# Optimization experiments

Hardware: AMD Instinct MI355X
Metric: run time of the kernel (lower is better)

The kernel has to match this reference:

```python
import jax, jax.numpy as jnp
import numpy as np

E, B, T, N, DIN = 8, 1024, 64, 16, 8
H, Z = 512, 128
DFLAT = T * N * DIN  # 8192


def setup_inputs() -> dict:
    key = jax.random.key(0)
    ks = jax.random.split(key, 10)
    def w(k, shape, fan_in):
        return jax.random.normal(k, shape, jnp.float32) * (1.0 / np.sqrt(fan_in))
    return {
        'x': jax.random.normal(ks[0], (B, T, N, DIN), jnp.float32),
        'eps': jax.random.normal(ks[1], (E, B, Z), jnp.float32),
        'enc_w1': w(ks[2], (E, DFLAT, H), DFLAT), 'enc_b1': jnp.zeros((E, H), jnp.float32),
        'enc_w2': w(ks[3], (E, H, H), H),         'enc_b2': jnp.zeros((E, H), jnp.float32),
        'mu_w':   w(ks[4], (E, H, Z), H),         'mu_b':   jnp.zeros((E, Z), jnp.float32),
        'lv_w':   w(ks[5], (E, H, Z), H),         'lv_b':   jnp.zeros((E, Z), jnp.float32),
        'dec_w1': w(ks[6], (E, Z, H), Z),         'dec_b1': jnp.zeros((E, H), jnp.float32),
        'dec_w2': w(ks[7], (E, H, H), H),         'dec_b2': jnp.zeros((E, H), jnp.float32),
        'dec_w3': w(ks[8], (E, H, DFLAT), H),     'dec_b3': jnp.zeros((E, DFLAT), jnp.float32),
    }


def _all_experts(x, eps, enc_w1, enc_b1, enc_w2, enc_b2, mu_w, mu_b, lv_w, lv_b,
                 dec_w1, dec_b1, dec_w2, dec_b2, dec_w3, dec_b3):
    # 'everyone_try_this_problem': every expert runs densely on the full batch.
    xf = x.reshape(x.shape[0], -1)                                            # [B, D]
    h = jax.nn.relu(jnp.einsum('bd,edh->ebh', xf, enc_w1) + enc_b1[:, None])  # [E, B, H]
    h = jax.nn.relu(jnp.einsum('ebh,ehk->ebk', h, enc_w2) + enc_b2[:, None])
    mu = jnp.einsum('ebh,ehz->ebz', h, mu_w) + mu_b[:, None]                  # [E, B, Z]
    logvar = jnp.einsum('ebh,ehz->ebz', h, lv_w) + lv_b[:, None]
    z = mu + jnp.exp(0.5 * logvar) * eps                                      # reparameterized sample
    hd = jax.nn.relu(jnp.einsum('ebz,ezh->ebh', z, dec_w1) + dec_b1[:, None])
    hd = jax.nn.relu(jnp.einsum('ebh,ehk->ebk', hd, dec_w2) + dec_b2[:, None])
    xhat = jnp.einsum('ebh,ehd->ebd', hd, dec_w3) + dec_b3[:, None]           # [E, B, D]
    losses = jnp.mean((xhat - xf[None]) ** 2, axis=-1)                        # [E, B] per-sample recon loss
    return mu, logvar, xhat, losses


def reference(x, eps, enc_w1, enc_b1, enc_w2, enc_b2, mu_w, mu_b, lv_w, lv_b,
              dec_w1, dec_b1, dec_w2, dec_b2, dec_w3, dec_b3):
    mu, logvar, xhat, losses = _all_experts(
        x, eps, enc_w1, enc_b1, enc_w2, enc_b2, mu_w, mu_b, lv_w, lv_b,
        dec_w1, dec_b1, dec_w2, dec_b2, dec_w3, dec_b3)
    # torch.min(all_loss[B,E], dim=1) -> argmin over experts (first-index tiebreak)
    expert_idx = jnp.argmin(losses, axis=0)                                   # [B]
    b = jnp.arange(x.shape[0])
    mu_sel = mu[expert_idx, b]                                                # [B, Z]
    logvar_sel = logvar[expert_idx, b]
    xhat_sel = xhat[expert_idx, b].reshape(x.shape)                           # [B, T, N, DIN]
    return mu_sel, logvar_sel, xhat_sel, expert_idx
```

## Files before the change

### kernel.cpp

```cpp
#include <hip/hip_runtime.h>

#define EE 8
#define BB 1024
#define DD 8192
#define HH 512
#define ZZ 128

typedef __attribute__((ext_vector_type(8))) short bf16x8;
typedef __attribute__((ext_vector_type(4))) float f32x4;
typedef __attribute__((address_space(1))) unsigned int u32g;
typedef __attribute__((address_space(3))) unsigned int u32l;

#define DEVI __device__ __forceinline__

DEVI float4 ld4(const float* p) { return *(const float4*)p; }

DEVI unsigned f2bf_u(float x) {
  unsigned u = __builtin_bit_cast(unsigned, x);
  return (u + 0x7FFFu + ((u >> 16) & 1u)) >> 16;
}
DEVI float bfu2f(unsigned h) { return __builtin_bit_cast(float, h << 16); }
DEVI float bf2f(short s) {
  return __builtin_bit_cast(float, ((unsigned)(unsigned short)s) << 16);
}
DEVI void split2(float x, short& hi, short& lo) {
  unsigned h = f2bf_u(x);
  hi = (short)h;
  lo = (short)f2bf_u(x - bfu2f(h));
}

DEVI void gload16(const void* g, void* l) {
  __builtin_amdgcn_global_load_lds((const u32g*)g, (u32l*)l, 16, 0, 0);
}

template <int ROWS, int WAVES>
DEVI void stageG(const short* src, int Kb, short* lds, int w, int laneoff) {
  const char* p = (const char*)src + laneoff;
  char* l = (char*)lds + w * 1024;
#pragma unroll
  for (int r = 0; r < ROWS / (WAVES * 8); ++r)
    gload16(p + (size_t)r * (WAVES * 8) * Kb, l + r * (WAVES * 1024));
}

template <int NPASS, int NF>
DEVI void mma_chunk(const char* Ah, const char* Al, const char* Bh, const char* Bl,
                    int abase, int bbase, f32x4 acc[4][NF]) {
#pragma unroll
  for (int kk = 0; kk < 2; ++kk) {
    const int kx = kk * 64;
    bf16x8 ah[4], al[4], bh[NF], bl[NF];
#pragma unroll
    for (int m = 0; m < 4; ++m) {
      ah[m] = *(const bf16x8*)(Ah + ((abase + m * 2048) ^ kx));
      if (NPASS == 3) al[m] = *(const bf16x8*)(Al + ((abase + m * 2048) ^ kx));
    }
#pragma unroll
    for (int n = 0; n < NF; ++n) {
      bh[n] = *(const bf16x8*)(Bh + ((bbase + n * 2048) ^ kx));
      if (NPASS == 3) bl[n] = *(const bf16x8*)(Bl + ((bbase + n * 2048) ^ kx));
    }
#pragma unroll
    for (int m = 0; m < 4; ++m)
#pragma unroll
      for (int n = 0; n < NF; ++n) {
        acc[m][n] = __builtin_amdgcn_mfma_f32_16x16x32_bf16(ah[m], bh[n], acc[m][n], 0, 0, 0);
        if (NPASS == 3) {
          acc[m][n] = __builtin_amdgcn_mfma_f32_16x16x32_bf16(ah[m], bl[n], acc[m][n], 0, 0, 0);
          acc[m][n] = __builtin_amdgcn_mfma_f32_16x16x32_bf16(al[m], bh[n], acc[m][n], 0, 0, 0);
        }
      }
  }
}

DEVI void mma_chunk256(const char* A, const char* B, int abase, int bbase,
                       f32x4 acc[8][4]) {
#pragma unroll
  for (int kk = 0; kk < 2; ++kk) {
    const int kx = kk * 64;
    bf16x8 ah[8], bh[4];
#pragma unroll
    for (int m = 0; m < 8; ++m) ah[m] = *(const bf16x8*)(A + ((abase + m * 2048) ^ kx));
#pragma unroll
    for (int n = 0; n < 4; ++n) bh[n] = *(const bf16x8*)(B + ((bbase + n * 2048) ^ kx));
#pragma unroll
    for (int m = 0; m < 8; ++m)
#pragma unroll
      for (int n = 0; n < 4; ++n)
        acc[m][n] = __builtin_amdgcn_mfma_f32_16x16x32_bf16(ah[m], bh[n], acc[m][n], 0, 0, 0);
  }
}

template <int NPASS, int NF, bool RELU, int OUT>
__global__ __launch_bounds__(256, (NPASS == 3 ? 2 : 3)) void gemm_k(
    const short* __restrict__ Ahg, const short* __restrict__ Alg,
    const short* __restrict__ Bhg, const short* __restrict__ Blg,
    const float* __restrict__ bias,
    float* __restrict__ Yf, short* __restrict__ Yh, short* __restrict__ Yl,
    int M, int N, int K, int APE, const int* __restrict__ cntPtr, int mSkip) {
  constexpr int BN = NF * 32;
  __shared__ short sA[(NPASS == 3 ? 2 : 1) * 128 * 64];
  __shared__ short sB[(NPASS == 3 ? 2 : 1) * BN * 64];
  const int e = blockIdx.z;
  const int m0 = blockIdx.y * 128, n0 = blockIdx.x * BN;
  if (m0 < mSkip) return;
  if (cntPtr) {
    if (m0 >= ((cntPtr[0] + 127) & ~127)) return;
  }
  const size_t eA = APE ? (size_t)e * M * K : 0;
  const short* Ae = Ahg + eA + (size_t)m0 * K;
  const short* Ale = (NPASS == 3) ? (Alg + eA + (size_t)m0 * K) : nullptr;
  const short* Be = Bhg + ((size_t)e * N + n0) * K;
  const short* Ble = (NPASS == 3) ? (Blg + ((size_t)e * N + n0) * K) : nullptr;

  const int t = threadIdx.x, w = t >> 6, lane = t & 63;
  const int wm = w >> 1, wn = w & 1;
  const int Kb = K * 2;
  const int laneoff = (w * 8 + (lane >> 3)) * Kb + (((lane & 7) ^ ((lane >> 3) & 7)) << 4);
  const int r16 = lane & 15, g = lane >> 4;
  const int c0 = ((g ^ (r16 & 7)) << 4);
  const int abase = (wm * 64 + r16) * 128 + c0;
  const int bbase = (wn * (NF * 16) + r16) * 128 + c0;

  f32x4 acc[4][NF];
#pragma unroll
  for (int m = 0; m < 4; ++m)
#pragma unroll
    for (int n = 0; n < NF; ++n) acc[m][n] = (f32x4){0.f, 0.f, 0.f, 0.f};

  for (int k0 = 0; k0 < K; k0 += 64) {
    stageG<128, 4>(Ae + k0, Kb, sA, w, laneoff);
    if (NPASS == 3) stageG<128, 4>(Ale + k0, Kb, sA + 128 * 64, w, laneoff);
    stageG<BN, 4>(Be + k0, Kb, sB, w, laneoff);
    if (NPASS == 3) stageG<BN, 4>(Ble + k0, Kb, sB + BN * 64, w, laneoff);
    __syncthreads();
    mma_chunk<NPASS, NF>((const char*)sA, (const char*)(sA + 128 * 64),
                         (const char*)sB, (const char*)(sB + BN * 64), abase, bbase, acc);
    __syncthreads();
  }

  const int col0 = n0 + wn * (NF * 16);
#pragma unroll
  for (int n = 0; n < NF; ++n) {
    const int cn = col0 + n * 16 + r16;
    const float bv = bias[(size_t)e * N + cn];
#pragma unroll
    for (int m = 0; m < 4; ++m)
#pragma unroll
      for (int r = 0; r < 4; ++r) {
        const int row = m0 + wm * 64 + m * 16 + g * 4 + r;
        float v = acc[m][n][r] + bv;
        if (RELU) v = fmaxf(v, 0.f);
        const size_t o = ((size_t)e * M + row) * N + cn;
        if (OUT == 0) {
          Yf[o] = v;
        } else {
          unsigned hb = f2bf_u(v);
          Yh[o] = (short)hb;
          if (NPASS == 3) Yl[o] = (short)f2bf_u(v - bfu2f(hb));
        }
      }
  }
}

__global__ __launch_bounds__(256, 4) void enc1_mainsplit_k(
    const short* __restrict__ Xhg, const short* __restrict__ Bhg,
    float* __restrict__ EncP) {
  __shared__ short sA[128 * 64];
  __shared__ short sB[64 * 64];
  const int raw = blockIdx.x;
  const int e = raw & 7;
  const int q = raw >> 3;
  const int m0 = (q & 7) * 128;
  const int ks = (q >> 3) & 1;
  const int n0 = (q >> 4) * 64;
  const int Kb = DD * 2;
  const short* Ae = Xhg + (size_t)m0 * DD;
  const short* Be = Bhg + ((size_t)e * HH + n0) * DD;

  const int t = threadIdx.x, w = t >> 6, lane = t & 63;
  const int wm = w >> 1, wn = w & 1;
  const int laneoff = (w * 8 + (lane >> 3)) * Kb + (((lane & 7) ^ ((lane >> 3) & 7)) << 4);
  const int r16 = lane & 15, g = lane >> 4;
  const int c0 = ((g ^ (r16 & 7)) << 4);
  const int abase = (wm * 64 + r16) * 128 + c0;
  const int bbase = (wn * 32 + r16) * 128 + c0;

  f32x4 acc[4][2];
#pragma unroll
  for (int m = 0; m < 4; ++m)
#pragma unroll
    for (int n = 0; n < 2; ++n) acc[m][n] = (f32x4){0.f, 0.f, 0.f, 0.f};

  const int kbeg = ks * 4096, kend = kbeg + 4096;
  for (int k0 = kbeg; k0 < kend; k0 += 64) {
    stageG<128, 4>(Ae + k0, Kb, sA, w, laneoff);
    stageG<64, 4>(Be + k0, Kb, sB, w, laneoff);
    __syncthreads();
    mma_chunk<1, 2>((const char*)sA, nullptr, (const char*)sB, nullptr,
                    abase, bbase, acc);
    __syncthreads();
  }

#pragma unroll
  for (int n = 0; n < 2; ++n) {
    const int cn = n0 + wn * 32 + n * 16 + r16;
#pragma unroll
    for (int m = 0; m < 4; ++m)
#pragma unroll
      for (int r = 0; r < 4; ++r) {
        const int row = m0 + wm * 64 + m * 16 + g * 4 + r;
        EncP[(((size_t)ks * EE + e) * BB + row) * HH + cn] = acc[m][n][r];
      }
  }
}

__global__ void fuse_enc1main_k(const float* __restrict__ EncP,
                                const float* __restrict__ enc_b1,
                                short* __restrict__ Hh) {
  const int idx = blockIdx.x * 256 + threadIdx.x;
  const size_t base = (size_t)idx * 8;
  float s[8];
  *(float4*)&s[0] = *(const float4*)&EncP[base];
  *(float4*)&s[4] = *(const float4*)&EncP[base + 4];
  {
    const float* p = EncP + (size_t)(EE * BB * HH) + base;
    float q[8];
    *(float4*)&q[0] = *(const float4*)p;
    *(float4*)&q[4] = *(const float4*)(p + 4);
#pragma unroll
    for (int j = 0; j < 8; ++j) s[j] += q[j];
  }
  const int e = (int)(base / (BB * HH));
  const int col = (int)(base % HH);
  short h8[8];
#pragma unroll
  for (int j = 0; j < 8; ++j) {
    const float v = fmaxf(s[j] + enc_b1[e * HH + col + j], 0.f);
    h8[j] = (short)f2bf_u(v);
  }
  *(bf16x8*)&Hh[base] = *(bf16x8*)h8;
}

__global__ __launch_bounds__(512, 2) void gemm_loss256_k(
    const short* __restrict__ Ahg, const short* __restrict__ Bhg,
    const float* __restrict__ bias, const short* __restrict__ xfh,
    float* __restrict__ partials) {
  __shared__ short sA[256 * 64];
  __shared__ short sB[256 * 64];
  __shared__ float red[256][4];
  int lin = blockIdx.x + 32 * (blockIdx.y + 4 * blockIdx.z);
  lin = (lin & 7) * 128 + (lin >> 3);
  const int bx = lin & 31, by = (lin >> 5) & 3, e = lin >> 7;
  const int m0 = by * 256, n0 = bx * 256;
  const int K = HH, Kb = HH * 2;
  const short* Ae = Ahg + ((size_t)e * BB + m0) * K;
  const short* Be = Bhg + ((size_t)e * DD + n0) * K;

  const int t = threadIdx.x, w = t >> 6, lane = t & 63;
  const int wm = w >> 2, wn = w & 3;
  const int laneoff = (w * 8 + (lane >> 3)) * Kb + (((lane & 7) ^ ((lane >> 3) & 7)) << 4);
  const int r16 = lane & 15, g = lane >> 4;
  const int c0 = ((g ^ (r16 & 7)) << 4);
  const int abase = (wm * 128 + r16) * 128 + c0;
  const int bbase = (wn * 64 + r16) * 128 + c0;

  f32x4 acc[8][4];
#pragma unroll
  for (int m = 0; m < 8; ++m)
#pragma unroll
    for (int n = 0; n < 4; ++n) acc[m][n] = (f32x4){0.f, 0.f, 0.f, 0.f};

  for (int k0 = 0; k0 < K; k0 += 64) {
    stageG<256, 8>(Ae + k0, Kb, sA, w, laneoff);
    stageG<256, 8>(Be + k0, Kb, sB, w, laneoff);
    __syncthreads();
    mma_chunk256((const char*)sA, (const char*)sB, abase, bbase, acc);
    __syncthreads();
  }

  float rs[8][4];
#pragma unroll
  for (int m = 0; m < 8; ++m)
#pragma unroll
    for (int r = 0; r < 4; ++r) rs[m][r] = 0.f;
#pragma unroll
  for (int n = 0; n < 4; ++n) {
    const int cn = n0 + wn * 64 + n * 16 + r16;
    const float bv = bias[(size_t)e * DD + cn];
#pragma unroll
    for (int m = 0; m < 8; ++m)
#pragma unroll
      for (int r = 0; r < 4; ++r) {
        const int row = m0 + wm * 128 + m * 16 + g * 4 + r;
        const float d = acc[m][n][r] + bv - bf2f(xfh[(size_t)row * DD + cn]);
        rs[m][r] = fmaf(d, d, rs[m][r]);
      }
  }
#pragma unroll
  for (int off = 1; off < 16; off <<= 1)
#pragma unroll
    for (int m = 0; m < 8; ++m)
#pragma unroll
      for (int r = 0; r < 4; ++r) rs[m][r] += __shfl_xor(rs[m][r], off);
  if (r16 == 0) {
#pragma unroll
    for (int m = 0; m < 8; ++m)
#pragma unroll
      for (int r = 0; r < 4; ++r) red[wm * 128 + m * 16 + g * 4 + r][wn] = rs[m][r];
  }
  __syncthreads();
  if (t < 256)
    partials[((size_t)e * BB + m0 + t) * 32 + bx] =
        red[t][0] + red[t][1] + red[t][2] + red[t][3];
}

template <int NPASS>
__global__ __launch_bounds__(256, 2) void gemm_loss_k(
    const short* __restrict__ Ahg, const short* __restrict__ Alg,
    const short* __restrict__ Bhg, const short* __restrict__ Blg,
    const float* __restrict__ bias, const float* __restrict__ xf,
    const int* __restrict__ rows, const int* __restrict__ cntPtr,
    float* __restrict__ partials, int K) {
  constexpr int NF = 4;
  __shared__ short sA[2 * 128 * 64];
  __shared__ short sB[2 * 128 * 64];
  __shared__ float red[128][2];
  const int e = blockIdx.z;
  const int m0 = blockIdx.y * 128, n0 = blockIdx.x * 128;
  int cntA = BB;
  if (cntPtr) {
    cntA = cntPtr[0];
    if (m0 >= ((cntA + 127) & ~127)) return;
  }
  const short* Ae = Ahg + ((size_t)e * BB + m0) * K;
  const short* Ale = Alg + ((size_t)e * BB + m0) * K;
  const short* Be = Bhg + ((size_t)e * DD + n0) * K;
  const short* Ble = Blg + ((size_t)e * DD + n0) * K;

  const int t = threadIdx.x, w = t >> 6, lane = t & 63;
  const int wm = w >> 1, wn = w & 1;
  const int Kb = K * 2;
  const int laneoff = (w * 8 + (lane >> 3)) * Kb + (((lane & 7) ^ ((lane >> 3) & 7)) << 4);
  const int r16 = lane & 15, g = lane >> 4;
  const int c0 = ((g ^ (r16 & 7)) << 4);
  const int abase = (wm * 64 + r16) * 128 + c0;
  const int bbase = (wn * 64 + r16) * 128 + c0;

  f32x4 acc[4][NF];
#pragma unroll
  for (int m = 0; m < 4; ++m)
#pragma unroll
    for (int n = 0; n < NF; ++n) acc[m][n] = (f32x4){0.f, 0.f, 0.f, 0.f};

  for (int k0 = 0; k0 < K; k0 += 64) {
    stageG<128, 4>(Ae + k0, Kb, sA, w, laneoff);
    stageG<128, 4>(Ale + k0, Kb, sA + 128 * 64, w, laneoff);
    stageG<128, 4>(Be + k0, Kb, sB, w, laneoff);
    stageG<128, 4>(Ble + k0, Kb, sB + 128 * 64, w, laneoff);
    __syncthreads();
    mma_chunk<NPASS, NF>((const char*)sA, (const char*)(sA + 128 * 64),
                         (const char*)sB, (const char*)(sB + 128 * 64), abase, bbase, acc);
    __syncthreads();
  }

  float rs[4][4];
#pragma unroll
  for (int m = 0; m < 4; ++m)
#pragma unroll
    for (int r = 0; r < 4; ++r) rs[m][r] = 0.f;
#pragma unroll
  for (int n = 0; n < NF; ++n) {
    const int cn = n0 + wn * 64 + n * 16 + r16;
    const float bv = bias[(size_t)e * DD + cn];
#pragma unroll
    for (int m = 0; m < 4; ++m)
#pragma unroll
      for (int r = 0; r < 4; ++r) {
        const int lrow = m0 + wm * 64 + m * 16 + g * 4 + r;
        const int xr = rows ? (lrow < cntA ? rows[lrow] : 0) : lrow;
        const float d = acc[m][n][r] + bv - xf[(size_t)xr * DD + cn];
        rs[m][r] = fmaf(d, d, rs[m][r]);
      }
  }
#pragma unroll
  for (int off = 1; off < 16; off <<= 1)
#pragma unroll
    for (int m = 0; m < 4; ++m)
#pragma unroll
      for (int r = 0; r < 4; ++r) rs[m][r] += __shfl_xor(rs[m][r], off);
  if (r16 == 0) {
#pragma unroll
    for (int m = 0; m < 4; ++m)
#pragma unroll
      for (int r = 0; r < 4; ++r) red[wm * 64 + m * 16 + g * 4 + r][wn] = rs[m][r];
  }
  __syncthreads();
  if (t < 128)
    partials[((size_t)e * BB + m0 + t) * 64 + blockIdx.x] = red[t][0] + red[t][1];
}

__global__ __launch_bounds__(512, 2) void gather_out256_k(
    const short* __restrict__ Ahg, const short* __restrict__ Bhg,
    const float* __restrict__ bias, const int* __restrict__ counts,
    const int* __restrict__ lists, float* __restrict__ out) {
  __shared__ short sA[256 * 64];
  __shared__ short sB[256 * 64];
  __shared__ int rows_s[256];
  const int e = blockIdx.z;
  const int cnt = counts[e];
  const int m0 = blockIdx.y * 256;
  if (m0 >= cnt) return;
  const int n0 = blockIdx.x * 256;
  const int K = HH, Kb = HH * 2;
  const short* Ae = Ahg + (size_t)e * BB * K;
  const short* Be = Bhg + ((size_t)e * DD + n0) * K;

  const int t = threadIdx.x, w = t >> 6, lane = t & 63;
  const int wm = w >> 2, wn = w & 3;
  const int csw16 = ((lane & 7) ^ ((lane >> 3) & 7)) << 4;
  const int laneoff = (w * 8 + (lane >> 3)) * Kb + csw16;
  const int r16 = lane & 15, g = lane >> 4;
  const int c0 = ((g ^ (r16 & 7)) << 4);
  const int abase = (wm * 128 + r16) * 128 + c0;
  const int bbase = (wn * 64 + r16) * 128 + c0;

  if (t < 256) rows_s[t] = (m0 + t < cnt) ? lists[e * BB + m0 + t] : -1;
  __syncthreads();
  int grow[4];
#pragma unroll
  for (int p = 0; p < 4; ++p) {
    int rr = rows_s[p * 64 + w * 8 + (lane >> 3)];
    grow[p] = rr < 0 ? 0 : rr;
  }

  f32x4 acc[8][4];
#pragma unroll
  for (int m = 0; m < 8; ++m)
#pragma unroll
    for (int n = 0; n < 4; ++n) acc[m][n] = (f32x4){0.f, 0.f, 0.f, 0.f};

  for (int k0 = 0; k0 < K; k0 += 64) {
#pragma unroll
    for (int p = 0; p < 4; ++p)
      gload16((const char*)Ae + (size_t)grow[p] * Kb + k0 * 2 + csw16,
              (char*)sA + p * 8192 + w * 1024);
    stageG<256, 8>(Be + k0, Kb, sB, w, laneoff);
    __syncthreads();
    mma_chunk256((const char*)sA, (const char*)sB, abase, bbase, acc);
    __syncthreads();
  }

#pragma unroll
  for (int n = 0; n < 4; ++n) {
    const int cn = n0 + wn * 64 + n * 16 + r16;
    const float bv = bias[(size_t)e * DD + cn];
#pragma unroll
    for (int m = 0; m < 8; ++m)
#pragma unroll
      for (int r = 0; r < 4; ++r) {
        const int rout = rows_s[wm * 128 + m * 16 + g * 4 + r];
        if (rout >= 0) out[(size_t)rout * DD + cn] = acc[m][n][r] + bv;
      }
  }
}

__global__ __launch_bounds__(256, 2) void enc1_pksplit_k(
    const short* __restrict__ Ahg, const short* __restrict__ Alg,
    const short* __restrict__ Bhg, const short* __restrict__ Blg,
    const int* __restrict__ cntPtr, float* __restrict__ PAf) {
  __shared__ short sA[2 * 128 * 64];
  __shared__ short sB[2 * 64 * 64];
  const int cnt = cntPtr[0];
  if (cnt == 0) return;
  const int m0 = blockIdx.y * 128;
  if (m0 >= ((cnt + 127) & ~127)) return;
  const int e = blockIdx.z;
  const int n0 = (blockIdx.x & 7) * 64;
  const int ks = blockIdx.x >> 3;
  const int Kb = DD * 2;
  const short* Ae = Ahg + (size_t)m0 * DD;
  const short* Ale = Alg + (size_t)m0 * DD;
  const short* Be = Bhg + ((size_t)e * HH + n0) * DD;
  const short* Ble = Blg + ((size_t)e * HH + n0) * DD;

  const int t = threadIdx.x, w = t >> 6, lane = t & 63;
  const int wm = w >> 1, wn = w & 1;
  const int laneoff = (w * 8 + (lane >> 3)) * Kb + (((lane & 7) ^ ((lane >> 3) & 7)) << 4);
  const int r16 = lane & 15, g = lane >> 4;
  const int c0 = ((g ^ (r16 & 7)) << 4);
  const int abase = (wm * 64 + r16) * 128 + c0;
  const int bbase = (wn * 32 + r16) * 128 + c0;

  f32x4 acc[4][2];
#pragma unroll
  for (int m = 0; m < 4; ++m)
#pragma unroll
    for (int n = 0; n < 2; ++n) acc[m][n] = (f32x4){0.f, 0.f, 0.f, 0.f};

  const int kbeg = ks * 1024, kend = kbeg + 1024;
  for (int k0 = kbeg; k0 < kend; k0 += 64) {
    stageG<128, 4>(Ae + k0, Kb, sA, w, laneoff);
    stageG<128, 4>(Ale + k0, Kb, sA + 128 * 64, w, laneoff);
    stageG<64, 4>(Be + k0, Kb, sB, w, laneoff);
    stageG<64, 4>(Ble + k0, Kb, sB + 64 * 64, w, laneoff);
    __syncthreads();
    mma_chunk<3, 2>((const char*)sA, (const char*)(sA + 128 * 64),
                    (const char*)sB, (const char*)(sB + 64 * 64), abase, bbase, acc);
    __syncthreads();
  }

#pragma unroll
  for (int n = 0; n < 2; ++n) {
    const int cn = n0 + wn * 32 + n * 16 + r16;
#pragma unroll
    for (int m = 0; m < 4; ++m)
#pragma unroll
      for (int r = 0; r < 4; ++r) {
        const int row = m0 + wm * 64 + m * 16 + g * 4 + r;
        PAf[(((size_t)ks * EE + e) * 256 + row) * HH + cn] = acc[m][n][r];
      }
  }
}

__global__ void fuse_enc1_k(const float* __restrict__ PAf,
                            const float* __restrict__ enc_b1,
                            const int* __restrict__ ambc,
                            short* __restrict__ PAh, short* __restrict__ PAl) {
  const int cnt = ambc[0];
  if (cnt == 0) return;
  const int cntPad = (cnt + 127) & ~127;
  const int idx = blockIdx.x * 256 + threadIdx.x;
  const size_t base = (size_t)idx * 8;
  const int e = (int)(base / (256 * HH));
  const int rem = (int)(base % (256 * HH));
  const int row = rem / HH;
  if (row >= cntPad) return;
  const int col = rem % HH;
  const size_t src = ((size_t)e * 256 + row) * HH + col;
  float s[8];
  *(float4*)&s[0] = *(const float4*)&PAf[src];
  *(float4*)&s[4] = *(const float4*)&PAf[src + 4];
#pragma unroll
  for (int ks = 1; ks < 8; ++ks) {
    const float* p = PAf + (size_t)ks * (EE * 256 * HH) + src;
    float q[8];
    *(float4*)&q[0] = *(const float4*)p;
    *(float4*)&q[4] = *(const float4*)(p + 4);
#pragma unroll
    for (int j = 0; j < 8; ++j) s[j] += q[j];
  }
  short h8[8], l8[8];
#pragma unroll
  for (int j = 0; j < 8; ++j) {
    const float v = fmaxf(s[j] + enc_b1[e * HH + col + j], 0.f);
    split2(v, h8[j], l8[j]);
  }
  const size_t o = ((size_t)e * BB + row) * HH + col;
  *(bf16x8*)&PAh[o] = *(bf16x8*)h8;
  *(bf16x8*)&PAl[o] = *(bf16x8*)l8;
}

__global__ void init_k(int* ambc) { ambc[0] = 0; }

__global__ void split_x_k(const float* __restrict__ x, short* __restrict__ Xh) {
  const int i = (blockIdx.x * 256 + threadIdx.x) * 8;
  float v[8];
  *(float4*)&v[0] = ld4(x + i);
  *(float4*)&v[4] = ld4(x + i + 4);
  short h[8];
#pragma unroll
  for (int j = 0; j < 8; ++j) h[j] = (short)f2bf_u(v[j]);
  *(bf16x8*)&Xh[i] = *(bf16x8*)h;
}

__global__ void biascat_k(const float* __restrict__ mu_b, const float* __restrict__ lv_b,
                          float* __restrict__ mlvB) {
  const int e = blockIdx.x, t = threadIdx.x;
  mlvB[e * 256 + t] = t < 128 ? mu_b[e * 128 + t] : lv_b[e * 128 + t - 128];
}

__global__ __launch_bounds__(256) void trans_split_k(
    const float* __restrict__ W, short* __restrict__ Th, short* __restrict__ Tl,
    int K, int N, int rowOff, int rowsPerE) {
  const int e = blockIdx.z;
  const int k0 = blockIdx.x * 64, n0 = blockIdx.y * 64;
  __shared__ float tile[64][65];
  const int t = threadIdx.x;
  const int tr = t >> 2, tc = (t & 3) * 16;
  const float* Wp = W + ((size_t)e * K + k0 + tr) * N + n0 + tc;
#pragma unroll
  for (int c = 0; c < 4; ++c) {
    float4 v = *(const float4*)(Wp + c * 4);
    tile[tr][tc + c * 4 + 0] = v.x;
    tile[tr][tc + c * 4 + 1] = v.y;
    tile[tr][tc + c * 4 + 2] = v.z;
    tile[tr][tc + c * 4 + 3] = v.w;
  }
  __syncthreads();
  short h8[16], l8[16];
#pragma unroll
  for (int j = 0; j < 16; ++j) split2(tile[tc + j][tr], h8[j], l8[j]);
  const size_t o = ((size_t)e * rowsPerE + rowOff + n0 + tr) * K + k0 + tc;
  *(bf16x8*)&Th[o] = *(bf16x8*)&h8[0];
  *(bf16x8*)&Th[o + 8] = *(bf16x8*)&h8[8];
  *(bf16x8*)&Tl[o] = *(bf16x8*)&l8[0];
  *(bf16x8*)&Tl[o + 8] = *(bf16x8*)&l8[8];
}

__global__ void z_k(const float* __restrict__ mlv, const float* __restrict__ eps,
                    short* __restrict__ Zh) {
  const int t = blockIdx.x * 256 + threadIdx.x;
  const int eb = t >> 7, z = t & 127;
  const float mu = mlv[(size_t)eb * 256 + z], lv = mlv[(size_t)eb * 256 + 128 + z];
  Zh[t] = (short)f2bf_u(fmaf(expf(0.5f * lv), eps[t], mu));
}

__global__ void zP_k(const float* __restrict__ mlvP, const float* __restrict__ eps,
                     const int* __restrict__ ambc, const int* __restrict__ amb,
                     short* __restrict__ ZgH, short* __restrict__ ZgL) {
  const int t = blockIdx.x * 256 + threadIdx.x;
  const int eb = t >> 7, z = t & 127;
  const int e = eb >> 10, i = eb & 1023;
  const int cntA = ambc[0];
  if (i >= ((cntA + 127) & ~127)) return;
  const int b = (i < cntA) ? amb[i] : 0;
  const float mu = mlvP[(size_t)eb * 256 + z], lv = mlvP[(size_t)eb * 256 + 128 + z];
  const float v = fmaf(expf(0.5f * lv), eps[((size_t)e * BB + b) * ZZ + z], mu);
  short h, l;
  split2(v, h, l);
  ZgH[t] = h;
  ZgL[t] = l;
}

__global__ void gather_x_k(const float* __restrict__ x, const int* __restrict__ ambc,
                           const int* __restrict__ amb, short* __restrict__ XgH,
                           short* __restrict__ XgL) {
  const int i = blockIdx.x;
  const int cntA = ambc[0];
  if (i >= ((cntA + 127) & ~127)) return;
  const int b = (i < cntA) ? amb[i] : 0;
  const float* xr = x + (size_t)b * DD;
  short* oh = XgH + (size_t)i * DD;
  short* ol = XgL + (size_t)i * DD;
  for (int j = threadIdx.x * 8; j < DD; j += 256 * 8) {
    float v[8];
    *(float4*)&v[0] = ld4(xr + j);
    *(float4*)&v[4] = ld4(xr + j + 4);
    short h[8], l[8];
#pragma unroll
    for (int q = 0; q < 8; ++q) split2(v[q], h[q], l[q]);
    *(bf16x8*)&oh[j] = *(bf16x8*)h;
    *(bf16x8*)&ol[j] = *(bf16x8*)l;
  }
}

__global__ void loss_reduce_k(const float* __restrict__ part, float* __restrict__ loss,
                              const int* __restrict__ cntPtr, int NBLK) {
  const int id = blockIdx.x * 256 + threadIdx.x;
  if (cntPtr) {
    if ((id & 1023) >= ((cntPtr[0] + 127) & ~127)) return;
  }
  const float* p = part + (size_t)id * NBLK;
  float s = 0.f;
  for (int j = 0; j < NBLK; ++j) s += p[j];
  loss[id] = s;
}

__global__ void argmin_flag_k(const float* __restrict__ loss, int* __restrict__ idx,
                              float* __restrict__ out_ix, int* __restrict__ ambc,
                              int* __restrict__ amb) {
  const int b = blockIdx.x * 256 + threadIdx.x;
  float best = loss[b], sec = 3.0e38f;
  int bi = 0;
#pragma unroll
  for (int e = 1; e < EE; ++e) {
    const float v = loss[e * BB + b];
    if (v < best) { sec = best; best = v; bi = e; }
    else if (v < sec) sec = v;
  }
  idx[b] = bi;
  out_ix[b] = (float)bi;
  if (sec - best < 10.0f + 0.001f * best) {
    int p = atomicAdd(ambc, 1);
    amb[p] = b;
  }
}

__global__ void fix_idx_k(const float* __restrict__ lossP, const int* __restrict__ ambc,
                          const int* __restrict__ amb, int* __restrict__ idx,
                          float* __restrict__ out_ix) {
  const int i = blockIdx.x * 256 + threadIdx.x;
  if (i >= ambc[0]) return;
  const int b = amb[i];
  float best = lossP[i];
  int bi = 0;
#pragma unroll
  for (int e = 1; e < EE; ++e) {
    const float v = lossP[e * 1024 + i];
    if (v < best) { best = v; bi = e; }
  }
  idx[b] = bi;
  out_ix[b] = (float)bi;
}

__global__ void select_k(const float* __restrict__ mlv, const int* __restrict__ idx,
                         float* __restrict__ out_mu, float* __restrict__ out_lv) {
  const int t = blockIdx.x * 256 + threadIdx.x;
  const int b = t >> 7, z = t & 127;
  const int e = idx[b];
  out_mu[t] = mlv[((size_t)(e * BB + b)) * 256 + z];
  out_lv[t] = mlv[((size_t)(e * BB + b)) * 256 + 128 + z];
}

__global__ void compact_k(const int* __restrict__ idx, int* __restrict__ counts,
                          int* __restrict__ lists) {
  __shared__ int cnt[EE];
  if (threadIdx.x < EE) cnt[threadIdx.x] = 0;
  __syncthreads();
  const int b = threadIdx.x;
  const int e = idx[b];
  const int pos = atomicAdd(&cnt[e], 1);
  lists[e * BB + pos] = b;
  __syncthreads();
  if (threadIdx.x < EE) counts[threadIdx.x] = cnt[threadIdx.x];
}

extern "C" void kernel_launch(void* const* d_in, const int* in_sizes, int n_in,
                              void* d_out, int out_size, void* d_ws, size_t ws_size,
                              hipStream_t stream) {
  const float* x      = (const float*)d_in[0];
  const float* eps    = (const float*)d_in[1];
  const float* enc_w1 = (const float*)d_in[2];
  const float* enc_b1 = (const float*)d_in[3];
  const float* enc_w2 = (const float*)d_in[4];
  const float* enc_b2 = (const float*)d_in[5];
  const float* mu_w   = (const float*)d_in[6];
  const float* mu_b   = (const float*)d_in[7];
  const float* lv_w   = (const float*)d_in[8];
  const float* lv_b   = (const float*)d_in[9];
  const float* dec_w1 = (const float*)d_in[10];
  const float* dec_b1 = (const float*)d_in[11];
  const float* dec_w2 = (const float*)d_in[12];
  const float* dec_b2 = (const float*)d_in[13];
  const float* dec_w3 = (const float*)d_in[14];
  const float* dec_b3 = (const float*)d_in[15];

  char* wsb = (char*)d_ws;
  size_t off = 0;
  auto alloc = [&](size_t bytes) -> void* {
    void* p = wsb + off;
    off = (off + bytes + 511) & ~(size_t)511;
    return p;
  };
  short* Xh    = (short*)alloc(16777216);
  short* ew1Th = (short*)alloc(67108864);
  short* ew1Tl = (short*)alloc(67108864);
  short* ew2Th = (short*)alloc(4194304);
  short* ew2Tl = (short*)alloc(4194304);
  short* mlvTh = (short*)alloc(2097152);
  short* mlvTl = (short*)alloc(2097152);
  short* dw1Th = (short*)alloc(1048576);
  short* dw1Tl = (short*)alloc(1048576);
  short* dw2Th = (short*)alloc(4194304);
  short* dw2Tl = (short*)alloc(4194304);
  short* dw3Th = (short*)alloc(67108864);
  short* dw3Tl = (short*)alloc(67108864);
  short* Hh    = (short*)alloc(8388608);
  short* H2h   = (short*)alloc(8388608);
  float* mlv   = (float*)alloc(8388608);
  float* mlvB  = (float*)alloc(8192);
  short* Zh    = (short*)alloc(2097152);
  float* part  = (float*)alloc(2097152);
  float* loss  = (float*)alloc(32768);
  int*   idx   = (int*)alloc(4096);
  int*   ambc  = (int*)alloc(512);
  int*   amb   = (int*)alloc(4096);
  int*   counts= (int*)alloc(512);
  int*   lists = (int*)alloc(4096);
  short* XgL   = (short*)alloc(16777216);
  short* PAh   = (short*)alloc(8388608);
  short* PAl   = (short*)alloc(8388608);
  short* PBh   = (short*)alloc(8388608);
  short* PBl   = (short*)alloc(8388608);
  float* mlvP  = (float*)alloc(8388608);
  short* ZgH   = (short*)alloc(2097152);
  short* ZgL   = (short*)alloc(2097152);
  float* lossP = (float*)alloc(32768);
  float* PAf   = (float*)alloc(33554432);
  short* XgH   = Xh;
  float* EncP  = (float*)XgL;

  float* out_mu = (float*)d_out;
  float* out_lv = out_mu + (size_t)BB * ZZ;
  float* out_xh = out_lv + (size_t)BB * ZZ;
  float* out_ix = out_xh + (size_t)BB * DD;

  const dim3 blk(256);

  init_k<<<1, 1, 0, stream>>>(ambc);
  split_x_k<<<4096, blk, 0, stream>>>(x, Xh);
  biascat_k<<<8, blk, 0, stream>>>(mu_b, lv_b, mlvB);
  trans_split_k<<<dim3(128, 8, 8), blk, 0, stream>>>(enc_w1, ew1Th, ew1Tl, 8192, 512, 0, 512);
  trans_split_k<<<dim3(8, 8, 8), blk, 0, stream>>>(enc_w2, ew2Th, ew2Tl, 512, 512, 0, 512);
  trans_split_k<<<dim3(8, 2, 8), blk, 0, stream>>>(mu_w, mlvTh, mlvTl, 512, 128, 0, 256);
  trans_split_k<<<dim3(8, 2, 8), blk, 0, stream>>>(lv_w, mlvTh, mlvTl, 512, 128, 128, 256);
  trans_split_k<<<dim3(2, 8, 8), blk, 0, stream>>>(dec_w1, dw1Th, dw1Tl, 128, 512, 0, 512);
  trans_split_k<<<dim3(8, 8, 8), blk, 0, stream>>>(dec_w2, dw2Th, dw2Tl, 512, 512, 0, 512);
  trans_split_k<<<dim3(8, 128, 8), blk, 0, stream>>>(dec_w3, dw3Th, dw3Tl, 512, 8192, 0, 8192);

  enc1_mainsplit_k<<<dim3(1024), blk, 0, stream>>>(Xh, ew1Th, EncP);
  fuse_enc1main_k<<<2048, blk, 0, stream>>>(EncP, enc_b1, Hh);
  gemm_k<1, 2, true, 1><<<dim3(8, 8, 8), blk, 0, stream>>>(
      Hh, nullptr, ew2Th, nullptr, enc_b2, nullptr, H2h, nullptr, 1024, 512, 512, 1, nullptr, 0);
  gemm_k<1, 2, false, 0><<<dim3(4, 8, 8), blk, 0, stream>>>(
      H2h, nullptr, mlvTh, nullptr, mlvB, mlv, nullptr, nullptr, 1024, 256, 512, 1, nullptr, 0);
  z_k<<<4096, blk, 0, stream>>>(mlv, eps, Zh);
  gemm_k<1, 2, true, 1><<<dim3(8, 8, 8), blk, 0, stream>>>(
      Zh, nullptr, dw1Th, nullptr, dec_b1, nullptr, Hh, nullptr, 1024, 512, 128, 1, nullptr, 0);
  gemm_k<1, 2, true, 1><<<dim3(8, 8, 8), blk, 0, stream>>>(
      Hh, nullptr, dw2Th, nullptr, dec_b2, nullptr, H2h, nullptr, 1024, 512, 512, 1, nullptr, 0);
  gemm_loss256_k<<<dim3(32, 4, 8), dim3(512), 0, stream>>>(
      H2h, dw3Th, dec_b3, Xh, part);
  loss_reduce_k<<<32, blk, 0, stream>>>(part, loss, nullptr, 32);
  argmin_flag_k<<<4, blk, 0, stream>>>(loss, idx, out_ix, ambc, amb);

  gather_x_k<<<1024, blk, 0, stream>>>(x, ambc, amb, XgH, XgL);
  enc1_pksplit_k<<<dim3(64, 2, 8), blk, 0, stream>>>(
      XgH, XgL, ew1Th, ew1Tl, ambc, PAf);
  fuse_enc1_k<<<512, blk, 0, stream>>>(PAf, enc_b1, ambc, PAh, PAl);
  gemm_k<3, 2, true, 1><<<dim3(8, 8, 8), blk, 0, stream>>>(
      XgH, XgL, ew1Th, ew1Tl, enc_b1, nullptr, PAh, PAl, 1024, 512, 8192, 0, ambc, 256);
  gemm_k<3, 2, true, 1><<<dim3(8, 8, 8), blk, 0, stream>>>(
      PAh, PAl, ew2Th, ew2Tl, enc_b2, nullptr, PBh, PBl, 1024, 512, 512, 1, ambc, 0);
  gemm_k<3, 2, false, 0><<<dim3(4, 8, 8), blk, 0, stream>>>(
      PBh, PBl, mlvTh, mlvTl, mlvB, mlvP, nullptr, nullptr, 1024, 256, 512, 1, ambc, 0);
  zP_k<<<4096, blk, 0, stream>>>(mlvP, eps, ambc, amb, ZgH, ZgL);
  gemm_k<3, 2, true, 1><<<dim3(8, 8, 8), blk, 0, stream>>>(
      ZgH, ZgL, dw1Th, dw1Tl, dec_b1, nullptr, PAh, PAl, 1024, 512, 128, 1, ambc, 0);
  gemm_k<3, 2, true, 1><<<dim3(8, 8, 8), blk, 0, stream>>>(
      PAh, PAl, dw2Th, dw2Tl, dec_b2, nullptr, PBh, PBl, 1024, 512, 512, 1, ambc, 0);
  gemm_loss_k<3><<<dim3(64, 8, 8), blk, 0, stream>>>(
      PBh, PBl, dw3Th, dw3Tl, dec_b3, x, amb, ambc, part, 512);
  loss_reduce_k<<<32, blk, 0, stream>>>(part, lossP, ambc, 64);
  fix_idx_k<<<4, blk, 0, stream>>>(lossP, ambc, amb, idx, out_ix);

  select_k<<<512, blk, 0, stream>>>(mlv, idx, out_mu, out_lv);
  compact_k<<<1, 1024, 0, stream>>>(idx, counts, lists);
  gather_out256_k<<<dim3(32, 4, 8), dim3(512), 0, stream>>>(
      H2h, dw3Th, dec_b3, counts, lists, out_xh);
}
```

Baseline: 643.9 us.

## Double-buffer LDS staging with K=32 chunks in the three main GEMM kernels

Turns the enc1 mainsplit, loss, and gather-output GEMMs from a single-buffer load-sync-compute-sync loop into a two-stage ping-pong. The next K=32 slab is issued with global_load_lds while MFMAs run on the current one. A combined vmcnt(0) wait plus barrier replaces the two syncthreads per step, so global-load latency is meant to overlap with compute. The XOR swizzle is dropped for a plain 64-byte row layout, which may add LDS bank conflicts on the bf16x8 reads and halves the MFMA work per barrier.

```diff
diff --git a/kernel.cpp b/kernel.cpp
--- a/kernel.cpp
+++ b/kernel.cpp
@@ -33,6 +33,13 @@
   __builtin_amdgcn_global_load_lds((const u32g*)g, (u32l*)l, 16, 0, 0);
 }
 
+DEVI void pipe_fence() {
+  __builtin_amdgcn_sched_barrier(0);
+  asm volatile("s_waitcnt vmcnt(0)" ::: "memory");
+  __builtin_amdgcn_s_barrier();
+  __builtin_amdgcn_sched_barrier(0);
+}
+
 template <int ROWS, int WAVES>
 DEVI void stageG(const short* src, int Kb, short* lds, int w, int laneoff) {
   const char* p = (const char*)src + laneoff;
@@ -40,6 +47,15 @@
 #pragma unroll
   for (int r = 0; r < ROWS / (WAVES * 8); ++r)
     gload16(p + (size_t)r * (WAVES * 8) * Kb, l + r * (WAVES * 1024));
+}
+
+template <int ROWS, int WAVES>
+DEVI void stage32(const short* src, int Kb, short* lds, int w, int laneoff32) {
+  const char* p = (const char*)src + laneoff32;
+  char* l = (char*)lds + w * 1024;
+#pragma unroll
+  for (int r = 0; r < ROWS / (WAVES * 16); ++r)
+    gload16(p + (size_t)r * (WAVES * 16) * Kb, l + r * (WAVES * 1024));
 }
 
 template <int NPASS, int NF>
@@ -72,22 +88,19 @@
   }
 }
 
-DEVI void mma_chunk256(const char* A, const char* B, int abase, int bbase,
-                       f32x4 acc[8][4]) {
-#pragma unroll
-  for (int kk = 0; kk < 2; ++kk) {
-    const int kx = kk * 64;
-    bf16x8 ah[8], bh[4];
-#pragma unroll
-    for (int m = 0; m < 8; ++m) ah[m] = *(const bf16x8*)(A + ((abase + m * 2048) ^ kx));
-#pragma unroll
-    for (int n = 0; n < 4; ++n) bh[n] = *(const bf16x8*)(B + ((bbase + n * 2048) ^ kx));
-#pragma unroll
-    for (int m = 0; m < 8; ++m)
-#pragma unroll
-      for (int n = 0; n < 4; ++n)
-        acc[m][n] = __builtin_amdgcn_mfma_f32_16x16x32_bf16(ah[m], bh[n], acc[m][n], 0, 0, 0);
-  }
+template <int NM, int NF>
+DEVI void mma32(const char* A, const char* B, int abase, int bbase,
+                f32x4 acc[NM][NF]) {
+  bf16x8 ah[NM], bh[NF];
+#pragma unroll
+  for (int m = 0; m < NM; ++m) ah[m] = *(const bf16x8*)(A + abase + m * 1024);
+#pragma unroll
+  for (int n = 0; n < NF; ++n) bh[n] = *(const bf16x8*)(B + bbase + n * 1024);
+#pragma unroll
+  for (int m = 0; m < NM; ++m)
+#pragma unroll
+    for (int n = 0; n < NF; ++n)
+      acc[m][n] = __builtin_amdgcn_mfma_f32_16x16x32_bf16(ah[m], bh[n], acc[m][n], 0, 0, 0);
 }
 
 template <int NPASS, int NF, bool RELU, int OUT>
@@ -165,8 +178,8 @@
 __global__ __launch_bounds__(256, 4) void enc1_mainsplit_k(
     const short* __restrict__ Xhg, const short* __restrict__ Bhg,
     float* __restrict__ EncP) {
-  __shared__ short sA[128 * 64];
-  __shared__ short sB[64 * 64];
+  __shared__ short sA[2][128 * 32];
+  __shared__ short sB[2][64 * 32];
   const int raw = blockIdx.x;
   const int e = raw & 7;
   const int q = raw >> 3;
@@ -179,11 +192,10 @@
 
   const int t = threadIdx.x, w = t >> 6, lane = t & 63;
   const int wm = w >> 1, wn = w & 1;
-  const int laneoff = (w * 8 + (lane >> 3)) * Kb + (((lane & 7) ^ ((lane >> 3) & 7)) << 4);
+  const int lo32 = (w * 16 + (lane >> 2)) * Kb + ((lane & 3) << 4);
   const int r16 = lane & 15, g = lane >> 4;
-  const int c0 = ((g ^ (r16 & 7)) << 4);
-  const int abase = (wm * 64 + r16) * 128 + c0;
-  const int bbase = (wn * 32 + r16) * 128 + c0;
+  const int abase = (wm * 64 + r16) * 64 + g * 16;
+  const int bbase = (wn * 32 + r16) * 64 + g * 16;
 
   f32x4 acc[4][2];
 #pragma unroll
@@ -191,14 +203,23 @@
 #pragma unroll
     for (int n = 0; n < 2; ++n) acc[m][n] = (f32x4){0.f, 0.f, 0.f, 0.f};
 
-  const int kbeg = ks * 4096, kend = kbeg + 4096;
-  for (int k0 = kbeg; k0 < kend; k0 += 64) {
-    stageG<128, 4>(Ae + k0, Kb, sA, w, laneoff);
-    stageG<64, 4>(Be + k0, Kb, sB, w, laneoff);
-    __syncthreads();
-    mma_chunk<1, 2>((const char*)sA, nullptr, (const char*)sB, nullptr,
-                    abase, bbase, acc);
-    __syncthreads();
+  const int kbeg = ks * 4096;
+  stage32<128, 4>(Ae + kbeg, Kb, sA[0], w, lo32);
+  stage32<64, 4>(Be + kbeg, Kb, sB[0], w, lo32);
+  pipe_fence();
+  for (int c = 0; c < 128; c += 2) {
+    if (c + 1 < 128) {
+      stage32<128, 4>(Ae + kbeg + (c + 1) * 32, Kb, sA[1], w, lo32);
+      stage32<64, 4>(Be + kbeg + (c + 1) * 32, Kb, sB[1], w, lo32);
+    }
+    mma32<4, 2>((const char*)sA[0], (const char*)sB[0], abase, bbase, acc);
+    pipe_fence();
+    if (c + 2 < 128) {
+      stage32<128, 4>(Ae + kbeg + (c + 2) * 32, Kb, sA[0], w, lo32);
+      stage32<64, 4>(Be + kbeg + (c + 2) * 32, Kb, sB[0], w, lo32);
+    }
+    mma32<4, 2>((const char*)sA[1], (const char*)sB[1], abase, bbase, acc);
+    pipe_fence();
   }
 
 #pragma unroll
@@ -245,24 +266,23 @@
     const short* __restrict__ Ahg, const short* __restrict__ Bhg,
     const float* __restrict__ bias, const short* __restrict__ xfh,
     float* __restrict__ partials) {
-  __shared__ short sA[256 * 64];
-  __shared__ short sB[256 * 64];
+  __shared__ short sA[2][256 * 32];
+  __shared__ short sB[2][256 * 32];
   __shared__ float red[256][4];
   int lin = blockIdx.x + 32 * (blockIdx.y + 4 * blockIdx.z);
   lin = (lin & 7) * 128 + (lin >> 3);
   const int bx = lin & 31, by = (lin >> 5) & 3, e = lin >> 7;
   const int m0 = by * 256, n0 = bx * 256;
-  const int K = HH, Kb = HH * 2;
-  const short* Ae = Ahg + ((size_t)e * BB + m0) * K;
-  const short* Be = Bhg + ((size_t)e * DD + n0) * K;
+  const int Kb = HH * 2;
+  const short* Ae = Ahg + ((size_t)e * BB + m0) * HH;
+  const short* Be = Bhg + ((size_t)e * DD + n0) * HH;
 
   const int t = threadIdx.x, w = t >> 6, lane = t & 63;
   const int wm = w >> 2, wn = w & 3;
-  const int laneoff = (w * 8 + (lane >> 3)) * Kb + (((lane & 7) ^ ((lane >> 3) & 7)) << 4);
+  const int lo32 = (w * 16 + (lane >> 2)) * Kb + ((lane & 3) << 4);
   const int r16 = lane & 15, g = lane >> 4;
-  const int c0 = ((g ^ (r16 & 7)) << 4);
-  const int abase = (wm * 128 + r16) * 128 + c0;
-  const int bbase = (wn * 64 + r16) * 128 + c0;
+  const int abase = (wm * 128 + r16) * 64 + g * 16;
+  const int bbase = (wn * 64 + r16) * 64 + g * 16;
 
   f32x4 acc[8][4];
 #pragma unroll
@@ -270,12 +290,22 @@
 #pragma unroll
     for (int n = 0; n < 4; ++n) acc[m][n] = (f32x4){0.f, 0.f, 0.f, 0.f};
 
-  for (int k0 = 0; k0 < K; k0 += 64) {
-    stageG<256, 8>(Ae + k0, Kb, sA, w, laneoff);
-    stageG<256, 8>(Be + k0, Kb, sB, w, laneoff);
-    __syncthreads();
-    mma_chunk256((const char*)sA, (const char*)sB, abase, bbase, acc);
-    __syncthreads();
+  stage32<256, 8>(Ae, Kb, sA[0], w, lo32);
+  stage32<256, 8>(Be, Kb, sB[0], w, lo32);
+  pipe_fence();
+  for (int c = 0; c < 16; c += 2) {
+    if (c + 1 < 16) {
+      stage32<256, 8>(Ae + (c + 1) * 32, Kb, sA[1], w, lo32);
+      stage32<256, 8>(Be + (c + 1) * 32, Kb, sB[1], w, lo32);
+    }
+    mma32<8, 4>((const char*)sA[0], (const char*)sB[0], abase, bbase, acc);
+    pipe_fence();
+    if (c + 2 < 16) {
+      stage32<256, 8>(Ae + (c + 2) * 32, Kb, sA[0], w, lo32);
+      stage32<256, 8>(Be + (c + 2) * 32, Kb, sB[0], w, lo32);
+    }
+    mma32<8, 4>((const char*)sA[1], (const char*)sB[1], abase, bbase, acc);
+    pipe_fence();
   }
 
   float rs[8][4];
@@ -403,35 +433,31 @@
     const short* __restrict__ Ahg, const short* __restrict__ Bhg,
     const float* __restrict__ bias, const int* __restrict__ counts,
     const int* __restrict__ lists, float* __restrict__ out) {
-  __shared__ short sA[256 * 64];
-  __shared__ short sB[256 * 64];
+  __shared__ short sA[2][256 * 32];
+  __shared__ short sB[2][256 * 32];
   __shared__ int rows_s[256];
   const int e = blockIdx.z;
   const int cnt = counts[e];
   const int m0 = blockIdx.y * 256;
   if (m0 >= cnt) return;
   const int n0 = blockIdx.x * 256;
-  const int K = HH, Kb = HH * 2;
-  const short* Ae = Ahg + (size_t)e * BB * K;
-  const short* Be = Bhg + ((size_t)e * DD + n0) * K;
+  const int Kb = HH * 2;
+  const short* Ae = Ahg + (size_t)e * BB * HH;
+  const short* Be = Bhg + ((size_t)e * DD + n0) * HH;
 
   const int t = threadIdx.x, w = t >> 6, lane = t & 63;
   const int wm = w >> 2, wn = w & 3;
-  const int csw16 = ((lane & 7) ^ ((lane >> 3) & 7)) << 4;
-  const int laneoff = (w * 8 + (lane >> 3)) * Kb + csw16;
+  const int lo32 = (w * 16 + (lane >> 2)) * Kb + ((lane & 3) << 4);
+  const int soff = (lane & 3) << 4;
   const int r16 = lane & 15, g = lane >> 4;
-  const int c0 = ((g ^ (r16 & 7)) << 4);
-  const int abase = (wm * 128 + r16) * 128 + c0;
-  const int bbase = (wn * 64 + r16) * 128 + c0;
+  const int abase = (wm * 128 + r16) * 64 + g * 16;
+  const int bbase = (wn * 64 + r16) * 64 + g * 16;
 
   if (t < 256) rows_s[t] = (m0 + t < cnt) ? lists[e * BB + m0 + t] : -1;
   __syncthreads();
-  int grow[4];
-#pragma unroll
-  for (int p = 0; p < 4; ++p) {
-    int rr = rows_s[p * 64 + w * 8 + (lane >> 3)];
-    grow[p] = rr < 0 ? 0 : rr;
-  }
+  const int r1 = w * 16 + (lane >> 2), r2 = r1 + 128;
+  int g1 = rows_s[r1]; g1 = g1 < 0 ? 0 : g1;
+  int g2 = rows_s[r2]; g2 = g2 < 0 ? 0 : g2;
 
   f32x4 acc[8][4];
 #pragma unroll
@@ -439,15 +465,29 @@
 #pragma unroll
     for (int n = 0; n < 4; ++n) acc[m][n] = (f32x4){0.f, 0.f, 0.f, 0.f};
 
-  for (int k0 = 0; k0 < K; k0 += 64) {
-#pragma unroll
-    for (int p = 0; p < 4; ++p)
-      gload16((const char*)Ae + (size_t)grow[p] * Kb + k0 * 2 + csw16,
-              (char*)sA + p * 8192 + w * 1024);
-    stageG<256, 8>(Be + k0, Kb, sB, w, laneoff);
-    __syncthreads();
-    mma_chunk256((const char*)sA, (const char*)sB, abase, bbase, acc);
-    __syncthreads();
+  auto STAGE_A = [&](int ke, short* dst) {
+    gload16((const char*)Ae + (size_t)g1 * Kb + (size_t)ke * 2 + soff,
+            (char*)dst + w * 1024);
+    gload16((const char*)Ae + (size_t)g2 * Kb + (size_t)ke * 2 + soff,
+            (char*)dst + 8192 + w * 1024);
+  };
+
+  STAGE_A(0, sA[0]);
+  stage32<256, 8>(Be, Kb, sB[0], w, lo32);
+  pipe_fence();
+  for (int c = 0; c < 16; c += 2) {
+    if (c + 1 < 16) {
+      STAGE_A((c + 1) * 32, sA[1]);
+      stage32<256, 8>(Be + (c + 1) * 32, Kb, sB[1], w, lo32);
+    }
+    mma32<8, 4>((const char*)sA[0], (const char*)sB[0], abase, bbase, acc);
+    pipe_fence();
+    if (c + 2 < 16) {
+      STAGE_A((c + 2) * 32, sA[0]);
+      stage32<256, 8>(Be + (c + 2) * 32, Kb, sB[0], w, lo32);
+    }
+    mma32<8, 4>((const char*)sA[1], (const char*)sB[1], abase, bbase, acc);
+    pipe_fence();
   }
 
 #pragma unroll
```

After: 656.7 us. No clear change (+2.0%).
